# Kernel tuning notes

Measured on AMD Instinct MI355X. Metric: run time of the kernel, lower is better.

Reference implementation:

```python
import jax, jax.numpy as jnp
import numpy as np

D = 256
H = 8

def setup_inputs() -> dict:
    key = jax.random.key(0)
    ks = jax.random.split(key, 6)
    b, n = 4, 2048
    X = jax.random.normal(ks[0], (b, n, D), dtype=jnp.float32)
    s = 1.0 / np.sqrt(D)
    Wq = jax.random.normal(ks[1], (D, D * H), dtype=jnp.float32) * s
    Wk = jax.random.normal(ks[2], (D, D * H), dtype=jnp.float32) * s
    Wv = jax.random.normal(ks[3], (D, D * H), dtype=jnp.float32) * s
    Wo = jax.random.normal(ks[4], (D * H, D), dtype=jnp.float32) * (1.0 / np.sqrt(D * H))
    bo = jnp.zeros((D,), dtype=jnp.float32)
    return {"X": X, "Wq": Wq, "Wk": Wk, "Wv": Wv, "Wo": Wo, "bo": bo}

def reference(X, Wq, Wk, Wv, Wo, bo):
    b, n, _ = X.shape
    scale = D ** (-0.25)
    # project and split heads: [b, n, H, D]
    q = (X @ Wq).reshape(b, n, H, D) * scale
    k = (X @ Wk).reshape(b, n, H, D) * scale
    v = (X @ Wv).reshape(b, n, H, D)
    # attention scores [b, H, n, n]
    scores = jnp.einsum("bqhd,bkhd->bhqk", q, k)
    attn = jax.nn.softmax(scores, axis=-1)
    out = jnp.einsum("bhqk,bkhd->bqhd", attn, v).reshape(b, n, H * D)
    return out @ Wo + bo
```

## Files before the change

### kernel.cpp

```cpp
#include <hip/hip_runtime.h>
#include <hip/hip_bf16.h>
#include <stdint.h>


using short8 = __attribute__((ext_vector_type(8))) short;
using f32x4  = __attribute__((ext_vector_type(4))) float;
using f32x16 = __attribute__((ext_vector_type(16))) float;

#define MFMA16(a, b, c) __builtin_amdgcn_mfma_f32_16x16x32_bf16((a), (b), (c), 0, 0, 0)
#define MFMA32(a, b, c) __builtin_amdgcn_mfma_f32_32x32x16_bf16((a), (b), (c), 0, 0, 0)

#if __has_builtin(__builtin_amdgcn_exp2f)
#define EXP2(x) __builtin_amdgcn_exp2f(x)
#else
#define EXP2(x) exp2f(x)
#endif

__device__ __forceinline__ uint16_t f2bf(float f) {
  union { float f; uint32_t u; } v; v.f = f;
  uint32_t u = v.u;
  u += 0x7fffu + ((u >> 16) & 1u);
  return (uint16_t)(u >> 16);
}

__device__ __forceinline__ uint32_t cvtpk_bf16(float lo, float hi) {
  uint32_t r;
  asm("v_cvt_pk_bf16_f32 %0, %1, %2" : "=v"(r) : "v"(lo), "v"(hi));
  return r;
}

__device__ __forceinline__ void swap32(uint32_t& a, uint32_t& b) {
  asm volatile("v_permlane32_swap_b32 %0, %1" : "+v"(a), "+v"(b));
}

__device__ __forceinline__ void gll16(const void* g, void* l) {
  __builtin_amdgcn_global_load_lds(
      (const __attribute__((address_space(1))) void*)g,
      (__attribute__((address_space(3))) void*)l, 16, 0, 0);
}

__global__ __launch_bounds__(256) void cast_x_k(const float* __restrict__ X,
                                                uint16_t* __restrict__ Xb, int n4) {
  int i = blockIdx.x * 256 + threadIdx.x;
  if (i >= n4) return;
  float4 v = ((const float4*)X)[i];
  union { uint16_t u[4]; uint2 p; } r;
  r.u[0] = f2bf(v.x); r.u[1] = f2bf(v.y); r.u[2] = f2bf(v.z); r.u[3] = f2bf(v.w);
  ((uint2*)Xb)[i] = r.p;
}

__global__ __launch_bounds__(256) void tcast_qkv_k(const float* __restrict__ Wq,
                                                   const float* __restrict__ Wk,
                                                   const float* __restrict__ Wv,
                                                   uint16_t* __restrict__ Wt3,
                                                   float qs) {
  __shared__ float T[64][65];
  const int R = 256, C = 2048;
  const int z = blockIdx.z;
  const float* W = (z == 0) ? Wq : (z == 1) ? Wk : Wv;
  const float scale = (z == 2) ? 1.0f : qs;
  uint16_t* Wt = Wt3 + (size_t)z * C * R;
  int c0 = blockIdx.x * 64, r0 = blockIdx.y * 64;
  int tid = threadIdx.x;
  int cc = tid & 63;
  for (int rr = tid >> 6; rr < 64; rr += 4)
    T[rr][cc] = W[(size_t)(r0 + rr) * C + c0 + cc];
  __syncthreads();
  int n = tid >> 2, kb = (tid & 3) * 16;
  uint16_t* orow = Wt + (size_t)(c0 + n) * R + r0 + kb;
#pragma unroll
  for (int j = 0; j < 16; ++j) orow[j] = f2bf(T[kb + j][n] * scale);
}

__global__ __launch_bounds__(256) void tcast_k(const float* __restrict__ W,
                                               uint16_t* __restrict__ Wt,
                                               int R, int C, float scale) {
  __shared__ float T[64][65];
  int c0 = blockIdx.x * 64, r0 = blockIdx.y * 64;
  int tid = threadIdx.x;
  int cc = tid & 63;
  for (int rr = tid >> 6; rr < 64; rr += 4)
    T[rr][cc] = W[(size_t)(r0 + rr) * C + c0 + cc];
  __syncthreads();
  int n = tid >> 2, kb = (tid & 3) * 16;
  uint16_t* orow = Wt + (size_t)(c0 + n) * R + r0 + kb;
#pragma unroll
  for (int j = 0; j < 16; ++j) orow[j] = f2bf(T[kb + j][n] * scale);
}

template <int EPI, int NT>
__global__ __launch_bounds__(256) void gemm_bt_k(const uint16_t* __restrict__ A,
                                                 const uint16_t* __restrict__ Bt,
                                                 void* __restrict__ Cv,
                                                 const float* __restrict__ bias,
                                                 int M, int N, int K) {
  __shared__ uint16_t As[128 * 64];
  __shared__ uint16_t Bs[NT * 32 * 64];
  const int tid = threadIdx.x;
  const int wv = tid >> 6, lane = tid & 63;
  const int ql = lane & 15, gq = lane >> 4;
  const int wr = wv >> 1, wc = wv & 1;
  const int m0 = blockIdx.y * 128, n0 = blockIdx.x * (NT * 32);

  f32x4 acc[4][NT];
#pragma unroll
  for (int i = 0; i < 4; ++i)
#pragma unroll
    for (int j = 0; j < NT; ++j) acc[i][j] = (f32x4){0.f, 0.f, 0.f, 0.f};

  const int nkb = K >> 6;
  for (int kb = 0; kb < nkb; ++kb) {
#pragma unroll
    for (int j = 0; j < 4; ++j) {
      int s = (wv * 4 + j) * 64 + lane;
      int row = s >> 3, c = s & 7;
      int gc = c ^ (row & 7);
      gll16(A + (size_t)(m0 + row) * K + kb * 64 + gc * 8, &As[(wv * 4 + j) * 512]);
    }
#pragma unroll
    for (int j = 0; j < NT; ++j) {
      int s = (wv * NT + j) * 64 + lane;
      int row = s >> 3, c = s & 7;
      int gc = c ^ (row & 7);
      gll16(Bt + (size_t)(n0 + row) * K + kb * 64 + gc * 8, &Bs[(wv * NT + j) * 512]);
    }
    __syncthreads();

    short8 af[4][2], bf[NT][2];
#pragma unroll
    for (int mt = 0; mt < 4; ++mt)
#pragma unroll
      for (int kk = 0; kk < 2; ++kk) {
        int row = wr * 64 + mt * 16 + ql;
        int c = (kk * 4 + gq) ^ (row & 7);
        af[mt][kk] = *(const short8*)&As[row * 64 + c * 8];
      }
#pragma unroll
    for (int nt = 0; nt < NT; ++nt)
#pragma unroll
      for (int kk = 0; kk < 2; ++kk) {
        int row = wc * (NT * 16) + nt * 16 + ql;
        int c = (kk * 4 + gq) ^ (row & 7);
        bf[nt][kk] = *(const short8*)&Bs[row * 64 + c * 8];
      }
#pragma unroll
    for (int kk = 0; kk < 2; ++kk)
#pragma unroll
      for (int mt = 0; mt < 4; ++mt)
#pragma unroll
        for (int nt = 0; nt < NT; ++nt)
          acc[mt][nt] = MFMA16(af[mt][kk], bf[nt][kk], acc[mt][nt]);
    __syncthreads();
  }

#pragma unroll
  for (int mt = 0; mt < 4; ++mt)
#pragma unroll
    for (int nt = 0; nt < NT; ++nt)
#pragma unroll
      for (int r = 0; r < 4; ++r) {
        int m = m0 + wr * 64 + mt * 16 + gq * 4 + r;
        int n = n0 + wc * (NT * 16) + nt * 16 + ql;
        float v = acc[mt][nt][r];
        if (EPI == 0) {
          ((uint16_t*)Cv)[(size_t)m * N + n] = f2bf(v);
        } else {
          ((float*)Cv)[(size_t)m * N + n] = v + bias[n];
        }
      }
}

__global__ __launch_bounds__(256, 2) void attn2_k(const uint16_t* __restrict__ qk,
                                                  const uint16_t* __restrict__ vtws,
                                                  uint16_t* __restrict__ ctx,
                                                  int b0, int nb) {
  __shared__ uint16_t Ks[2][32 * 256];
  __shared__ uint16_t Vts[2][256 * 32];
  const int S = 2048;
  const int h = blockIdx.x & 7;
  const int t = blockIdx.x >> 3;
  const int bb = t >> 4, qb = t & 15;
  const int tid = threadIdx.x, w = tid >> 6, lane = tid & 63;
  const int l31 = lane & 31, hi = lane >> 5;
  const size_t SN = (size_t)nb * S;

  short8 qf[16];
  {
    const uint16_t* qrow =
        qk + (size_t)(bb * S + qb * 128 + w * 32 + l31) * 4096 + h * 256 + hi * 8;
#pragma unroll
    for (int ds = 0; ds < 16; ++ds) qf[ds] = *(const short8*)(qrow + ds * 16);
  }

  uint32_t ok[4], ov[4];
#pragma unroll
  for (int j = 0; j < 4; ++j) {
    int s = (j * 4 + w) * 64 + lane;
    int krw = s >> 5, kc = s & 31;
    int kgc = kc ^ krw;
    ok[j] = (uint32_t)(((bb * S + krw) * 4096 + 2048 + h * 256 + kgc * 8) * 2);
    int d = s >> 2, vc = s & 3;
    int cg = vc ^ ((d >> 1) & 3);
    ov[j] = (uint32_t)((((h * 256 + d) * SN) + (size_t)bb * S + cg * 8) * 2);
  }
  const uint32_t kstep = 32 * 4096 * 2;
  const uint32_t vstep = 32 * 2;

  const char* kgbase = (const char*)qk;
  const char* vgbase = (const char*)vtws;

  auto stageK = [&](int buf, int kb) {
#pragma unroll
    for (int j = 0; j < 4; ++j)
      gll16(kgbase + ok[j] + (uint32_t)kb * kstep, &Ks[buf][(j * 4 + w) * 512]);
  };
  auto stageV = [&](int buf, int kb) {
#pragma unroll
    for (int j = 0; j < 4; ++j)
      gll16(vgbase + ov[j] + (uint32_t)kb * vstep, &Vts[buf][(j * 4 + w) * 512]);
  };

  f32x16 cacc[8];
#pragma unroll
  for (int db = 0; db < 8; ++db)
#pragma unroll
    for (int r = 0; r < 16; ++r) cacc[db][r] = 0.f;
  float m_run = -3e38f, l_run = 0.f;
  short8 pa0, pa1;

  const int kx = l31 << 4;
  const int vx = ((l31 >> 1) & 3) << 4;
  const int hi16 = hi << 4;

  f32x16 sA;

  auto qk_only = [&](int cur) {
    const char* kr = (const char*)Ks[cur] + l31 * 512;
#pragma unroll
    for (int r = 0; r < 16; ++r) sA[r] = 0.f;
    __builtin_amdgcn_s_setprio(1);
#pragma unroll
    for (int i = 0; i < 16; ++i) {
      int off = (i * 32 + hi16) ^ kx;
      sA = MFMA32(*(const short8*)(kr + off), qf[i], sA);
    }
    __builtin_amdgcn_s_setprio(0);
  };

  auto qk_pv = [&](int cur) {
    const char* kr = (const char*)Ks[cur] + l31 * 512;
    const char* vb = (const char*)Vts[cur ^ 1];
#pragma unroll
    for (int r = 0; r < 16; ++r) sA[r] = 0.f;
    __builtin_amdgcn_s_setprio(1);
#pragma unroll
    for (int i = 0; i < 16; ++i) {
      int off = (i * 32 + hi16) ^ kx;
      sA = MFMA32(*(const short8*)(kr + off), qf[i], sA);
      const int ks = i >> 3, db = i & 7;
      int voff = ((ks * 2 + hi) << 4) ^ vx;
      short8 vf = *(const short8*)(vb + (db * 32 + l31) * 64 + voff);
      cacc[db] = MFMA32(ks ? pa1 : pa0, vf, cacc[db]);
    }
    __builtin_amdgcn_s_setprio(0);
  };

  auto pv_only = [&](int slot) {
    const char* vb = (const char*)Vts[slot];
    __builtin_amdgcn_s_setprio(1);
#pragma unroll
    for (int ks = 0; ks < 2; ++ks) {
      int voff = ((ks * 2 + hi) << 4) ^ vx;
      short8 p = ks ? pa1 : pa0;
#pragma unroll
      for (int db = 0; db < 8; ++db) {
        short8 vf = *(const short8*)(vb + (db * 32 + l31) * 64 + voff);
        cacc[db] = MFMA32(p, vf, cacc[db]);
      }
    }
    __builtin_amdgcn_s_setprio(0);
  };

  auto sm_pack = [&]() {
    float pm = fmaxf(
        fmaxf(fmaxf(fmaxf(sA[0], sA[1]), fmaxf(sA[2], sA[3])),
              fmaxf(fmaxf(sA[4], sA[5]), fmaxf(sA[6], sA[7]))),
        fmaxf(fmaxf(fmaxf(sA[8], sA[9]), fmaxf(sA[10], sA[11])),
              fmaxf(fmaxf(sA[12], sA[13]), fmaxf(sA[14], sA[15]))));
    pm = fmaxf(pm, __shfl_xor(pm, 32));

    if (__any(pm - m_run > 8.0f)) {
      float mn = fmaxf(m_run, pm);
      float al = EXP2(m_run - mn);
      m_run = mn;
      l_run *= al;
#pragma unroll
      for (int r = 0; r < 16; ++r) {
        float a = __shfl(al, (r & 3) + 8 * (r >> 2) + 4 * hi);
#pragma unroll
        for (int db = 0; db < 8; ++db) cacc[db][r] *= a;
      }
    }

    float ps = 0.f;
#pragma unroll
    for (int r = 0; r < 16; ++r) { sA[r] = EXP2(sA[r] - m_run); ps += sA[r]; }
    ps += __shfl_xor(ps, 32);
    l_run += ps;

    uint32_t W[4][2];
#pragma unroll
    for (int g = 0; g < 4; ++g) {
      W[g][0] = cvtpk_bf16(sA[4 * g], sA[4 * g + 1]);
      W[g][1] = cvtpk_bf16(sA[4 * g + 2], sA[4 * g + 3]);
    }
    swap32(W[0][0], W[1][0]); swap32(W[0][1], W[1][1]);
    swap32(W[2][0], W[3][0]); swap32(W[2][1], W[3][1]);
    union U { uint32_t u[4]; short8 v; };
    U a0, a1;
    a0.u[0] = W[0][0]; a0.u[1] = W[0][1]; a0.u[2] = W[1][0]; a0.u[3] = W[1][1];
    a1.u[0] = W[2][0]; a1.u[1] = W[2][1]; a1.u[2] = W[3][0]; a1.u[3] = W[3][1];
    pa0 = a0.v; pa1 = a1.v;
  };

  stageK(0, 0);
  __syncthreads();

  stageK(1, 1);
  stageV(0, 0);
  qk_only(0);
  sm_pack();
  __syncthreads();

  for (int tt = 1; tt < 64; ++tt) {
    const int cur = tt & 1;
    if (tt < 63) stageK(cur ^ 1, tt + 1);
    stageV(cur, tt);
    qk_pv(cur);
    sm_pack();
    __syncthreads();
  }
  pv_only(1);

  float linv = 1.f / l_run;
  uint16_t* crow = ctx + (size_t)((b0 + bb) * S + qb * 128 + w * 32) * 2048 + h * 256;
#pragma unroll
  for (int r = 0; r < 16; ++r) {
    int qr = (r & 3) + 8 * (r >> 2) + 4 * hi;
    float lr = __shfl(linv, qr);
#pragma unroll
    for (int db = 0; db < 8; ++db)
      crow[(size_t)qr * 2048 + db * 32 + l31] = f2bf(cacc[db][r] * lr);
  }
}

extern "C" void kernel_launch(void* const* d_in, const int* in_sizes, int n_in,
                              void* d_out, int out_size, void* d_ws, size_t ws_size,
                              hipStream_t stream) {
  const float* X  = (const float*)d_in[0];
  const float* Wq = (const float*)d_in[1];
  const float* Wk = (const float*)d_in[2];
  const float* Wv = (const float*)d_in[3];
  const float* Wo = (const float*)d_in[4];
  const float* bo = (const float*)d_in[5];
  float* out = (float*)d_out;

  const int B = 4, S = 2048, Dm = 256, DH = 2048;
  (void)in_sizes; (void)n_in; (void)out_size; (void)ws_size;

  uint16_t* p = (uint16_t*)d_ws;
  uint16_t* Xb  = p; p += (size_t)B * S * Dm;
  uint16_t* Wqt = p; p += (size_t)DH * Dm;
  uint16_t* Wkt = p; p += (size_t)DH * Dm;
  uint16_t* Wvt = p; p += (size_t)DH * Dm;
  uint16_t* Wot = p; p += (size_t)Dm * DH;
  uint16_t* ctx = p; p += (size_t)B * S * DH;
  uint16_t* qkw = p; p += (size_t)B * S * (2 * DH);
  uint16_t* vtws = p;
  (void)Wkt; (void)Wvt;

  const float qs = 0.25f * 1.2011224087864498f;

  cast_x_k<<<dim3((B * S * Dm / 4 + 255) / 256), 256, 0, stream>>>(X, Xb, B * S * Dm / 4);
  tcast_qkv_k<<<dim3(DH / 64, Dm / 64, 3), 256, 0, stream>>>(Wq, Wk, Wv, Wqt, qs);
  tcast_k<<<dim3(Dm / 64, DH / 64), 256, 0, stream>>>(Wo, Wot, DH, Dm, 1.0f);

  gemm_bt_k<0, 4><<<dim3((2 * DH) / 128, (B * S) / 128), 256, 0, stream>>>(
      Xb, Wqt, qkw, nullptr, B * S, 2 * DH, Dm);
  gemm_bt_k<0, 4><<<dim3((B * S) / 128, DH / 128), 256, 0, stream>>>(
      Wvt, Xb, vtws, nullptr, DH, B * S, Dm);
  attn2_k<<<dim3(512), 256, 0, stream>>>(qkw, vtws, ctx, 0, B);
  gemm_bt_k<1, 2><<<dim3(Dm / 64, (B * S) / 128), 256, 0, stream>>>(
      ctx, Wot, out, bo, B * S, Dm, DH);
}
```

Measured before the change: 259.5 us.

## Triple-buffer K tiles and use partial vmcnt waits in attention loop

The attention kernel's K shared-memory buffer grows from two to three slots, so K tiles are prefetched two iterations ahead. Each full __syncthreads is replaced by an s_waitcnt vmcnt(4) plus barrier, which leaves the newest K load in flight across the barrier instead of draining every global-to-LDS load. The goal is to hide global load latency behind the QK and PV MFMA work. In exchange, LDS use per block rises to about 80 KB, which tightens the limit on two resident blocks per CU, and correctness now depends on exact load counts in flight.

```diff
diff --git a/kernel.cpp b/kernel.cpp
--- a/kernel.cpp
+++ b/kernel.cpp
@@ -174,7 +174,7 @@
                                                   const uint16_t* __restrict__ vtws,
                                                   uint16_t* __restrict__ ctx,
                                                   int b0, int nb) {
-  __shared__ uint16_t Ks[2][32 * 256];
+  __shared__ uint16_t Ks[3][32 * 256];
   __shared__ uint16_t Vts[2][256 * 32];
   const int S = 2048;
   const int h = blockIdx.x & 7;
@@ -209,15 +209,17 @@
   const char* kgbase = (const char*)qk;
   const char* vgbase = (const char*)vtws;
 
-  auto stageK = [&](int buf, int kb) {
+  auto stageK = [&](int u) {
+    uint16_t* dst = Ks[u % 3];
 #pragma unroll
     for (int j = 0; j < 4; ++j)
-      gll16(kgbase + ok[j] + (uint32_t)kb * kstep, &Ks[buf][(j * 4 + w) * 512]);
-  };
-  auto stageV = [&](int buf, int kb) {
+      gll16(kgbase + ok[j] + (uint32_t)u * kstep, &dst[(j * 4 + w) * 512]);
+  };
+  auto stageV = [&](int u) {
+    uint16_t* dst = Vts[u & 1];
 #pragma unroll
     for (int j = 0; j < 4; ++j)
-      gll16(vgbase + ov[j] + (uint32_t)kb * vstep, &Vts[buf][(j * 4 + w) * 512]);
+      gll16(vgbase + ov[j] + (uint32_t)u * vstep, &dst[(j * 4 + w) * 512]);
   };
 
   f32x16 cacc[8];
@@ -234,8 +236,8 @@
 
   f32x16 sA;
 
-  auto qk_only = [&](int cur) {
-    const char* kr = (const char*)Ks[cur] + l31 * 512;
+  auto qk_only = [&](int kslot) {
+    const char* kr = (const char*)Ks[kslot] + l31 * 512;
 #pragma unroll
     for (int r = 0; r < 16; ++r) sA[r] = 0.f;
     __builtin_amdgcn_s_setprio(1);
@@ -247,9 +249,9 @@
     __builtin_amdgcn_s_setprio(0);
   };
 
-  auto qk_pv = [&](int cur) {
-    const char* kr = (const char*)Ks[cur] + l31 * 512;
-    const char* vb = (const char*)Vts[cur ^ 1];
+  auto qk_pv = [&](int kslot, int vslot) {
+    const char* kr = (const char*)Ks[kslot] + l31 * 512;
+    const char* vb = (const char*)Vts[vslot];
 #pragma unroll
     for (int r = 0; r < 16; ++r) sA[r] = 0.f;
     __builtin_amdgcn_s_setprio(1);
@@ -265,8 +267,8 @@
     __builtin_amdgcn_s_setprio(0);
   };
 
-  auto pv_only = [&](int slot) {
-    const char* vb = (const char*)Vts[slot];
+  auto pv_only = [&](int vslot) {
+    const char* vb = (const char*)Vts[vslot];
     __builtin_amdgcn_s_setprio(1);
 #pragma unroll
     for (int ks = 0; ks < 2; ++ks) {
@@ -323,24 +325,32 @@
     pa0 = a0.v; pa1 = a1.v;
   };
 
-  stageK(0, 0);
-  __syncthreads();
-
-  stageK(1, 1);
-  stageV(0, 0);
+#define WAITBAR(N)                                             \
+  do {                                                         \
+    asm volatile("s_waitcnt vmcnt(" #N ")" ::: "memory");      \
+    __builtin_amdgcn_s_barrier();                              \
+  } while (0)
+
+  stageK(0);
+  stageK(1);
+  WAITBAR(4);
+
+  stageV(0);
+  stageK(2);
   qk_only(0);
   sm_pack();
-  __syncthreads();
+  WAITBAR(4);
 
   for (int tt = 1; tt < 64; ++tt) {
-    const int cur = tt & 1;
-    if (tt < 63) stageK(cur ^ 1, tt + 1);
-    stageV(cur, tt);
-    qk_pv(cur);
+    stageV(tt);
+    if (tt <= 61) stageK(tt + 2);
+    qk_pv(tt % 3, (tt - 1) & 1);
     sm_pack();
-    __syncthreads();
+    if (tt <= 61) { WAITBAR(4); }
+    else          { WAITBAR(0); }
   }
   pv_only(1);
+#undef WAITBAR
 
   float linv = 1.f / l_run;
   uint16_t* crow = ctx + (size_t)((b0 + bb) * S + qb * 128 + w * 32) * 2048 + h * 256;
@@ -377,7 +387,7 @@
   uint16_t* ctx = p; p += (size_t)B * S * DH;
   uint16_t* qkw = p; p += (size_t)B * S * (2 * DH);
   uint16_t* vtws = p;
-  (void)Wkt; (void)Wvt;
+  (void)Wkt;
 
   const float qs = 0.25f * 1.2011224087864498f;
 
```

After: 306.2 us. 1.18x slower.
